# Performance work log

Hardware: AMD Instinct MI355X
Metric: run time of the kernel (lower is better)

Reference implementation:

```python
import jax, jax.numpy as jnp
import numpy as np

N, F, H, C, E = 100000, 128, 64, 16, 1000000


def _prop(x, src, dst, w):
    # gather source features, scale by edge weight, scatter-add to destinations
    msgs = x[src] * w[:, None]  # [E, H]
    return jax.ops.segment_sum(msgs, dst, num_segments=N)


def _gru(x, h, W_ih, W_hh, b_ih, b_hh):
    gi = x @ W_ih.T + b_ih  # [N, 3H]
    gh = h @ W_hh.T + b_hh
    i_r, i_z, i_n = jnp.split(gi, 3, axis=1)
    h_r, h_z, h_n = jnp.split(gh, 3, axis=1)
    r = jax.nn.sigmoid(i_r + h_r)
    z = jax.nn.sigmoid(i_z + h_z)
    n = jnp.tanh(i_n + r * h_n)
    return (1.0 - z) * n + z * h


def setup_inputs() -> dict:
    key = jax.random.key(0)
    ks = jax.random.split(key, 20)
    s = 0.05
    inp = {
        'x': jax.random.normal(ks[0], (N, F), jnp.float32),
        'edge_index': jax.random.randint(ks[1], (2, E), 0, N),
        'edge_weight': jax.random.uniform(ks[2], (E,), jnp.float32),
        'edge_index_re': jax.random.randint(ks[3], (2, E), 0, N),
        'edge_weight_re': jax.random.uniform(ks[4], (E,), jnp.float32),
        'W_first': jax.random.normal(ks[5], (H, F), jnp.float32) * s,
        'b_first': jnp.zeros((H,), jnp.float32),
        'W_con1': jax.random.normal(ks[6], (H, 2 * H), jnp.float32) * s,
        'b_con1': jnp.zeros((H,), jnp.float32),
        'W_con2': jax.random.normal(ks[7], (H, 2 * H), jnp.float32) * s,
        'b_con2': jnp.zeros((H,), jnp.float32),
        'W_lin1': jax.random.normal(ks[8], (H, H), jnp.float32) * s,
        'b_lin1': jnp.zeros((H,), jnp.float32),
        'W_out': jax.random.normal(ks[9], (C, H), jnp.float32) * s,
        'b_out': jnp.zeros((C,), jnp.float32),
        'W_ih': jax.random.normal(ks[10], (3 * H, H), jnp.float32) * s,
        'W_hh': jax.random.normal(ks[11], (3 * H, H), jnp.float32) * s,
        'b_ih': jnp.zeros((3 * H,), jnp.float32),
        'b_hh': jnp.zeros((3 * H,), jnp.float32),
    }
    return inp


def reference(x, edge_index, edge_weight, edge_index_re, edge_weight_re,
              W_first, b_first, W_con1, b_con1, W_con2, b_con2,
              W_lin1, b_lin1, W_out, b_out, W_ih, W_hh, b_ih, b_hh):
    src, dst = edge_index[0], edge_index[1]
    src_r, dst_r = edge_index_re[0], edge_index_re[1]

    x = x @ W_first.T + b_first  # [N, H]; dropout is identity at inference
    h = x

    x1 = _prop(x, src, dst, edge_weight)
    x2 = _prop(x, src_r, dst_r, edge_weight_re)
    x = jnp.concatenate([x1, x2], axis=1) @ W_con1.T + b_con1
    x = _gru(x, h, W_ih, W_hh, b_ih, b_hh)
    x = x @ W_lin1.T + b_lin1

    x1 = _prop(x, src, dst, edge_weight)
    x2 = _prop(x, src_r, dst_r, edge_weight_re)
    x = jnp.concatenate([x1, x2], axis=1) @ W_con2.T + b_con2
    x = _gru(x, h, W_ih, W_hh, b_ih, b_hh)
    x = x @ W_out.T + b_out
    return jax.nn.log_softmax(x, axis=-1)
```

## Files before the change

### kernel.cpp

```cpp
#include <hip/hip_runtime.h>

#define NN 100000
#define FF 128
#define HH 64
#define CC 16
#define EE 1000000
#define NSEG (2*NN)
#define BSH 11
#define BKD  (1 << BSH)
#define NBUK ((NSEG + BKD - 1) / BKD)
#define EPB 4096
#define P1BLK ((2*EE + EPB - 1) / EPB)

typedef __bf16 bf16;
typedef __attribute__((ext_vector_type(8))) __bf16 bf16x8;
typedef __attribute__((ext_vector_type(4))) __bf16 bf16x4;
typedef __attribute__((ext_vector_type(4))) float f32x4;

__device__ __forceinline__ float fsig(float t)  { return 1.0f/(1.0f+__expf(-t)); }
__device__ __forceinline__ float ftanh(float t) { return 1.0f - 2.0f/(__expf(2.0f*t)+1.0f); }

__device__ __forceinline__ unsigned pack_sw(int s, float w) {
    unsigned short u = __builtin_bit_cast(unsigned short, (bf16)w);
    return ((unsigned)s << 15) | (u & 0x7FFFu);
}

__global__ void precomp_kernel(const float* __restrict__ W_ih, const float* __restrict__ b_ih,
                               const float* __restrict__ Wc1,  const float* __restrict__ bc1,
                               const float* __restrict__ Wc2,  const float* __restrict__ bc2,
                               const float* __restrict__ W_hh, const float* __restrict__ W_first,
                               const float* __restrict__ W_lin1, const float* __restrict__ W_out,
                               bf16* __restrict__ W1bf, float* __restrict__ b1,
                               bf16* __restrict__ W2bf, float* __restrict__ b2,
                               bf16* __restrict__ Whbf, bf16* __restrict__ Wfbf,
                               bf16* __restrict__ Wlbf, bf16* __restrict__ Wobf)
{
    int idx = blockIdx.x*blockDim.x + threadIdx.x;
    const int t0 = 192*128;
    const int t1 = t0 + 192;
    const int t2 = t1 + 192*64;
    const int t3 = t2 + 64*128;
    const int t4 = t3 + 64*64;
    const int t5 = t4 + 16*64;
    if (idx < t0) {
        int j = idx >> 7, k = idx & 127;
        float s1 = 0.f, s2 = 0.f;
        for (int m=0; m<64; ++m) {
            float wih = W_ih[j*64+m];
            s1 += wih * Wc1[m*128+k];
            s2 += wih * Wc2[m*128+k];
        }
        W1bf[idx] = (bf16)s1; W2bf[idx] = (bf16)s2;
    } else if (idx < t1) {
        int j = idx - t0;
        float s1 = b_ih[j], s2 = b_ih[j];
        for (int m=0; m<64; ++m) {
            float wih = W_ih[j*64+m];
            s1 += wih * bc1[m];
            s2 += wih * bc2[m];
        }
        b1[j] = s1; b2[j] = s2;
    } else if (idx < t2) {
        int i = idx - t1;  Whbf[i] = (bf16)W_hh[i];
    } else if (idx < t3) {
        int i = idx - t2;  Wfbf[i] = (bf16)W_first[i];
    } else if (idx < t4) {
        int i = idx - t3;  Wlbf[i] = (bf16)W_lin1[i];
    } else if (idx < t5) {
        int i = idx - t4;  Wobf[i] = (bf16)W_out[i];
    }
}


__global__ __launch_bounds__(256) void bucket_count_kernel(const int* __restrict__ ei,
                                                           const int* __restrict__ ei_re,
                                                           int* __restrict__ bkcnt)
{
    __shared__ int hist[NBUK];
    const int t = threadIdx.x;
    for (int i=t; i<NBUK; i+=256) hist[i] = 0;
    __syncthreads();
    const long e0 = (long)blockIdx.x * EPB;
    #pragma unroll
    for (int it=0; it<16; ++it) {
        long e = e0 + it*256 + t;
        int d = -1;
        if (e < EE)        d = ei[EE + e];
        else if (e < 2*EE) d = NN + ei_re[EE + (e - EE)];
        if (d >= 0) atomicAdd(&hist[d >> BSH], 1);
    }
    __syncthreads();
    for (int i=t; i<NBUK; i+=256) if (hist[i]) atomicAdd(&bkcnt[i], hist[i]);
}

__global__ void bucket_scan_kernel(const int* __restrict__ bkcnt,
                                   int* __restrict__ bkbase, int* __restrict__ bkcur,
                                   int* __restrict__ rp)
{
    if (threadIdx.x == 0) {
        int acc = 0;
        for (int i=0; i<NBUK; ++i) { bkbase[i] = acc; bkcur[i] = acc; acc += bkcnt[i]; }
        bkbase[NBUK] = acc;
        rp[NSEG] = 2*EE;
    }
}

__global__ __launch_bounds__(256) void fillA_kernel(const int* __restrict__ ei,
                                                    const float* __restrict__ ew,
                                                    const int* __restrict__ ei_re,
                                                    const float* __restrict__ ew_re,
                                                    int* __restrict__ bkcur,
                                                    int* __restrict__ tmp_d,
                                                    unsigned* __restrict__ tmp_p)
{
    __shared__ int hist[NBUK];
    __shared__ int base[NBUK];
    const int t = threadIdx.x;
    for (int i=t; i<NBUK; i+=256) hist[i] = 0;
    __syncthreads();
    const long e0 = (long)blockIdx.x * EPB;
    int pr[16];
    #pragma unroll
    for (int it=0; it<16; ++it) {
        long e = e0 + it*256 + t;
        int d = -1;
        if (e < EE)        d = ei[EE + e];
        else if (e < 2*EE) d = NN + ei_re[EE + (e - EE)];
        if (d >= 0) {
            int b = d >> BSH;
            int r = atomicAdd(&hist[b], 1);
            pr[it] = (b << 16) | r;
        } else pr[it] = -1;
    }
    __syncthreads();
    for (int i=t; i<NBUK; i+=256) base[i] = atomicAdd(&bkcur[i], hist[i]);
    __syncthreads();
    #pragma unroll
    for (int it=0; it<16; ++it) {
        if (pr[it] < 0) continue;
        long e = e0 + it*256 + t;
        int d, s; float w;
        if (e < EE) { d = ei[EE+e]; s = ei[e]; w = ew[e]; }
        else { long j = e - EE; d = NN + ei_re[EE+j]; s = ei_re[j]; w = ew_re[j]; }
        int pos = base[pr[it] >> 16] + (pr[it] & 0xFFFF);
        tmp_d[pos] = d;
        tmp_p[pos] = pack_sw(s, w);
    }
}

__global__ __launch_bounds__(1024) void fillB_kernel(const int* __restrict__ bkbase,
                                                     const int* __restrict__ tmp_d,
                                                     const unsigned* __restrict__ tmp_p,
                                                     unsigned* __restrict__ edata,
                                                     int* __restrict__ rp)
{
    __shared__ int cntL[BKD];
    __shared__ int scanL[1024];
    const int t  = threadIdx.x;
    const int b  = blockIdx.x;
    const int d0 = b << BSH;
    const int dn = min(BKD, NSEG - d0);
    const int p0 = bkbase[b];
    const int p1 = bkbase[b+1];
    for (int i=t; i<BKD; i+=1024) cntL[i] = 0;
    __syncthreads();
    for (int pos = p0 + t; pos < p1; pos += 1024)
        atomicAdd(&cntL[tmp_d[pos] - d0], 1);
    __syncthreads();
    int a0 = cntL[2*t], a1 = cntL[2*t+1];
    int ps = a0 + a1;
    scanL[t] = ps;
    __syncthreads();
    #pragma unroll
    for (int off=1; off<1024; off<<=1) {
        int x = (t>=off) ? scanL[t-off] : 0;
        __syncthreads();
        scanL[t] += x;
        __syncthreads();
    }
    int g0 = p0 + scanL[t] - ps;
    int g1 = g0 + a0;
    if (2*t   < dn) rp[d0 + 2*t]   = g0;
    if (2*t+1 < dn) rp[d0 + 2*t+1] = g1;
    cntL[2*t]   = g0;
    cntL[2*t+1] = g1;
    __syncthreads();
    for (int pos = p0 + t; pos < p1; pos += 1024) {
        int d = tmp_d[pos];
        int p = atomicAdd(&cntL[d - d0], 1);
        edata[p] = tmp_p[pos];
    }
}

__global__ __launch_bounds__(256) void csr_prop_kernel(const bf16* __restrict__ X,
    const int* __restrict__ rp, const unsigned* __restrict__ edata,
    bf16* __restrict__ x1, bf16* __restrict__ x2)
{
    int s = blockIdx.x*4 + (threadIdx.x>>6);
    if (s >= NSEG) return;
    const int lane = threadIdx.x & 63;
    const int q  = lane >> 4;
    const int fl = lane & 15;
    const int e0 = rp[s], e1 = rp[s+1];
    float a0=0.f, a1=0.f, a2=0.f, a3=0.f;
    for (int base = e0; base < e1; base += 16) {
        unsigned pk[4]; float vw[4];
        #pragma unroll
        for (int j=0;j<4;++j) {
            int e = base + j*4 + q;
            unsigned p = edata[e < e1 ? e : e0];
            pk[j] = p;
            vw[j] = (e < e1) ? __uint_as_float((p & 0x7FFFu) << 16) : 0.f;
        }
        bf16x4 xv[4];
        #pragma unroll
        for (int j=0;j<4;++j)
            xv[j] = *(const bf16x4*)&X[(long)(pk[j] >> 15)*HH + 4*fl];
        #pragma unroll
        for (int j=0;j<4;++j) {
            a0 += vw[j]*(float)xv[j][0];
            a1 += vw[j]*(float)xv[j][1];
            a2 += vw[j]*(float)xv[j][2];
            a3 += vw[j]*(float)xv[j][3];
        }
    }
    a0 += __shfl_xor(a0, 32); a0 += __shfl_xor(a0, 16);
    a1 += __shfl_xor(a1, 32); a1 += __shfl_xor(a1, 16);
    a2 += __shfl_xor(a2, 32); a2 += __shfl_xor(a2, 16);
    a3 += __shfl_xor(a3, 32); a3 += __shfl_xor(a3, 16);
    if (q == 0) {
        bf16* o = (s < NN) ? &x1[(long)s*HH] : &x2[(long)(s-NN)*HH];
        bf16x4 ov = {(bf16)a0, (bf16)a1, (bf16)a2, (bf16)a3};
        *(bf16x4*)&o[4*fl] = ov;
    }
}


__global__ __launch_bounds__(256, 2) void lin_first_mfma_kernel(
    const float* __restrict__ X, const bf16* __restrict__ Wf,
    const float* __restrict__ b, float* __restrict__ Y, bf16* __restrict__ Ybf)
{
    const int t = threadIdx.x;
    const int w = t >> 6, lane = t & 63, col = lane & 15, quad = lane >> 4;
    bf16x8 B[4];
    #pragma unroll
    for (int ks=0; ks<4; ++ks)
        B[ks] = *(const bf16x8*)&Wf[(16*w+col)*128 + ks*32 + quad*8];
    const float bv = b[16*w + col];
    __shared__ bf16 Alds[32][136];
    const int m_st = t >> 3, c_in = t & 7;
    for (int tb = blockIdx.x*32; tb < NN; tb += gridDim.x*32) {
        const float4* rx = (const float4*)&X[(long)(tb+m_st)*FF];
        #pragma unroll
        for (int it=0; it<4; ++it) {
            int cc = c_in + it*8;
            float4 v = rx[cc];
            bf16x4 bvv = {(bf16)v.x,(bf16)v.y,(bf16)v.z,(bf16)v.w};
            *(bf16x4*)&Alds[m_st][cc*4] = bvv;
        }
        __syncthreads();
        f32x4 acc[2] = {{0.f,0.f,0.f,0.f},{0.f,0.f,0.f,0.f}};
        #pragma unroll
        for (int ks=0; ks<4; ++ks)
            #pragma unroll
            for (int mt=0; mt<2; ++mt) {
                bf16x8 a = *(const bf16x8*)&Alds[mt*16+col][ks*32+quad*8];
                acc[mt] = __builtin_amdgcn_mfma_f32_16x16x32_bf16(a, B[ks], acc[mt], 0,0,0);
            }
        __syncthreads();
        #pragma unroll
        for (int mt=0; mt<2; ++mt)
            #pragma unroll
            for (int r=0; r<4; ++r) {
                long n = tb + mt*16 + quad*4 + r;
                float val = acc[mt][r] + bv;
                Y  [n*HH + 16*w+col] = val;
                Ybf[n*HH + 16*w+col] = (bf16)val;
            }
    }
}

__global__ __launch_bounds__(256, 2) void lin64_mfma_kernel(
    const float* __restrict__ X, const bf16* __restrict__ Wl,
    const float* __restrict__ b, bf16* __restrict__ Ybf)
{
    const int t = threadIdx.x;
    const int w = t >> 6, lane = t & 63, col = lane & 15, quad = lane >> 4;
    bf16x8 B[2];
    #pragma unroll
    for (int ks=0; ks<2; ++ks)
        B[ks] = *(const bf16x8*)&Wl[(16*w+col)*64 + ks*32 + quad*8];
    const float bv = b[16*w + col];
    __shared__ bf16 Alds[32][72];
    const int m_st = t >> 3, c_in = t & 7;
    for (int tb = blockIdx.x*32; tb < NN; tb += gridDim.x*32) {
        const float4* rx = (const float4*)&X[(long)(tb+m_st)*HH];
        #pragma unroll
        for (int it=0; it<2; ++it) {
            int cc = c_in + it*8;
            float4 v = rx[cc];
            bf16x4 bvv = {(bf16)v.x,(bf16)v.y,(bf16)v.z,(bf16)v.w};
            *(bf16x4*)&Alds[m_st][cc*4] = bvv;
        }
        __syncthreads();
        f32x4 acc[2] = {{0.f,0.f,0.f,0.f},{0.f,0.f,0.f,0.f}};
        #pragma unroll
        for (int ks=0; ks<2; ++ks)
            #pragma unroll
            for (int mt=0; mt<2; ++mt) {
                bf16x8 a = *(const bf16x8*)&Alds[mt*16+col][ks*32+quad*8];
                acc[mt] = __builtin_amdgcn_mfma_f32_16x16x32_bf16(a, B[ks], acc[mt], 0,0,0);
            }
        __syncthreads();
        #pragma unroll
        for (int mt=0; mt<2; ++mt)
            #pragma unroll
            for (int r=0; r<4; ++r)
                Ybf[(long)(tb+mt*16+quad*4+r)*HH + 16*w+col] = (bf16)(acc[mt][r] + bv);
    }
}

__global__ __launch_bounds__(256) void out_mfma_kernel(
    const float* __restrict__ X, const bf16* __restrict__ Wo,
    const float* __restrict__ b, float* __restrict__ Y)
{
    const int t = threadIdx.x;
    const int w = t >> 6, lane = t & 63, col = lane & 15, quad = lane >> 4;
    bf16x8 B[2];
    #pragma unroll
    for (int ks=0; ks<2; ++ks)
        B[ks] = *(const bf16x8*)&Wo[col*64 + ks*32 + quad*8];
    const float bv = b[col];
    __shared__ bf16 Alds[128][72];
    const int r_st = t >> 1, sub = t & 1;
    const int tb = blockIdx.x*128;
    {
        const float4* rx = (const float4*)&X[(long)(tb+r_st)*HH];
        #pragma unroll
        for (int it=0; it<8; ++it) {
            int cc = sub*8 + it;
            float4 v = rx[cc];
            bf16x4 bvv = {(bf16)v.x,(bf16)v.y,(bf16)v.z,(bf16)v.w};
            *(bf16x4*)&Alds[r_st][cc*4] = bvv;
        }
    }
    __syncthreads();
    f32x4 acc[2] = {{0.f,0.f,0.f,0.f},{0.f,0.f,0.f,0.f}};
    #pragma unroll
    for (int ks=0; ks<2; ++ks)
        #pragma unroll
        for (int mt=0; mt<2; ++mt) {
            bf16x8 a = *(const bf16x8*)&Alds[w*32 + mt*16 + col][ks*32+quad*8];
            acc[mt] = __builtin_amdgcn_mfma_f32_16x16x32_bf16(a, B[ks], acc[mt], 0,0,0);
        }
    #pragma unroll
    for (int mt=0; mt<2; ++mt) {
        #pragma unroll
        for (int r=0; r<4; ++r) {
            int n = tb + w*32 + mt*16 + quad*4 + r;
            float val = acc[mt][r] + bv;
            float m = val;
            #pragma unroll
            for (int off=8; off>0; off>>=1) m = fmaxf(m, __shfl_xor(m, off, 16));
            float ex = __expf(val - m);
            float s = ex;
            #pragma unroll
            for (int off=8; off>0; off>>=1) s += __shfl_xor(s, off, 16);
            if (n < NN) Y[(long)n*CC + col] = val - m - __logf(s);
        }
    }
}

__global__ __launch_bounds__(256, 2) void layer_mfma_kernel(
    const bf16* __restrict__ X1, const bf16* __restrict__ X2,
    const float* __restrict__ H,
    const bf16* __restrict__ Wg, const float* __restrict__ bg,
    const bf16* __restrict__ Wh, const float* __restrict__ bh,
    float* __restrict__ Hout)
{
    const int t    = threadIdx.x;
    const int w    = t >> 6;
    const int lane = t & 63;
    const int col  = lane & 15;
    const int quad = lane >> 4;

    bf16x8 Bg[3][4];
    bf16x8 Bh[3][2];
    float bgv[3], bhv[3];
    #pragma unroll
    for (int jt=0; jt<3; ++jt) {
        int J = jt*64 + 16*w + col;
        #pragma unroll
        for (int ks=0; ks<4; ++ks)
            Bg[jt][ks] = *(const bf16x8*)&Wg[J*128 + ks*32 + quad*8];
        #pragma unroll
        for (int ks=0; ks<2; ++ks)
            Bh[jt][ks] = *(const bf16x8*)&Wh[J*64 + ks*32 + quad*8];
        bgv[jt] = bg[J];
        bhv[jt] = bh[J];
    }

    __shared__ bf16 Alds[32][200];

    const int m_st = t >> 3;
    const int c_in = t & 7;

    for (int tb = blockIdx.x*32; tb < NN; tb += gridDim.x*32) {
        {
            long n = tb + m_st;
            *(bf16x8*)&Alds[m_st][c_in*8]      = *(const bf16x8*)&X1[n*HH + c_in*8];
            *(bf16x8*)&Alds[m_st][64 + c_in*8] = *(const bf16x8*)&X2[n*HH + c_in*8];
            const float4* rh = (const float4*)&H[n*HH];
            float4 a = rh[c_in*2], b4 = rh[c_in*2+1];
            bf16x8 hb = {(bf16)a.x,(bf16)a.y,(bf16)a.z,(bf16)a.w,
                         (bf16)b4.x,(bf16)b4.y,(bf16)b4.z,(bf16)b4.w};
            *(bf16x8*)&Alds[m_st][128 + c_in*8] = hb;
        }
        __syncthreads();

        f32x4 accg[2][3];
        f32x4 acch[2][3];
        #pragma unroll
        for (int mt=0; mt<2; ++mt)
            #pragma unroll
            for (int jt=0; jt<3; ++jt) {
                accg[mt][jt] = (f32x4){0.f,0.f,0.f,0.f};
                acch[mt][jt] = (f32x4){0.f,0.f,0.f,0.f};
            }

        #pragma unroll
        for (int ks=0; ks<4; ++ks) {
            #pragma unroll
            for (int mt=0; mt<2; ++mt) {
                bf16x8 a = *(const bf16x8*)&Alds[mt*16 + col][ks*32 + quad*8];
                #pragma unroll
                for (int jt=0; jt<3; ++jt)
                    accg[mt][jt] = __builtin_amdgcn_mfma_f32_16x16x32_bf16(
                        a, Bg[jt][ks], accg[mt][jt], 0, 0, 0);
            }
        }
        #pragma unroll
        for (int ks=0; ks<2; ++ks) {
            #pragma unroll
            for (int mt=0; mt<2; ++mt) {
                bf16x8 a = *(const bf16x8*)&Alds[mt*16 + col][128 + ks*32 + quad*8];
                #pragma unroll
                for (int jt=0; jt<3; ++jt)
                    acch[mt][jt] = __builtin_amdgcn_mfma_f32_16x16x32_bf16(
                        a, Bh[jt][ks], acch[mt][jt], 0, 0, 0);
            }
        }
        __syncthreads();

        const int c = 16*w + col;
        #pragma unroll
        for (int mt=0; mt<2; ++mt) {
            #pragma unroll
            for (int r=0; r<4; ++r) {
                long n = tb + mt*16 + quad*4 + r;
                float gr = accg[mt][0][r] + bgv[0];
                float gz = accg[mt][1][r] + bgv[1];
                float gn = accg[mt][2][r] + bgv[2];
                float hr = acch[mt][0][r] + bhv[0];
                float hz = acch[mt][1][r] + bhv[1];
                float hn = acch[mt][2][r] + bhv[2];
                float rr = fsig(gr + hr);
                float zz = fsig(gz + hz);
                float nv = ftanh(gn + rr*hn);
                float hv = H[n*HH + c];
                Hout[n*HH + c] = (1.0f - zz)*nv + zz*hv;
            }
        }
    }
}

extern "C" void kernel_launch(void* const* d_in, const int* in_sizes, int n_in,
                              void* d_out, int out_size, void* d_ws, size_t ws_size,
                              hipStream_t stream)
{
    const float* x       = (const float*)d_in[0];
    const int*   ei      = (const int*)  d_in[1];
    const float* ew      = (const float*)d_in[2];
    const int*   ei_re   = (const int*)  d_in[3];
    const float* ew_re   = (const float*)d_in[4];
    const float* W_first = (const float*)d_in[5];
    const float* b_first = (const float*)d_in[6];
    const float* W_con1  = (const float*)d_in[7];
    const float* b_con1  = (const float*)d_in[8];
    const float* W_con2  = (const float*)d_in[9];
    const float* b_con2  = (const float*)d_in[10];
    const float* W_lin1  = (const float*)d_in[11];
    const float* b_lin1  = (const float*)d_in[12];
    const float* W_out   = (const float*)d_in[13];
    const float* b_out   = (const float*)d_in[14];
    const float* W_ih    = (const float*)d_in[15];
    const float* W_hh    = (const float*)d_in[16];
    const float* b_ih    = (const float*)d_in[17];
    const float* b_hh    = (const float*)d_in[18];
    float* out = (float*)d_out;

    float* h    = (float*)d_ws;
    float* hA   = h  + (long)NN*HH;
    bf16*  x1b  = (bf16*)(hA + (long)NN*HH);
    bf16*  x2b  = x1b + (long)NN*HH;
    bf16*  hbf  = x2b + (long)NN*HH;
    bf16*  hAbf = hbf + (long)NN*HH;
    float* b1 = (float*)(hAbf + (long)NN*HH);
    float* b2 = b1 + 192;
    bf16*  W1bf = (bf16*)(b2 + 192);
    bf16*  W2bf = W1bf + 192*128;
    bf16*  Whbf = W2bf + 192*128;
    bf16*  Wfbf = Whbf + 192*64;
    bf16*  Wlbf = Wfbf + 64*128;
    bf16*  Wobf = Wlbf + 64*64;
    int*   rp     = (int*)(Wobf + 16*64);
    int*   bkcnt  = rp + NSEG + 1;
    int*   bkbase = bkcnt + NBUK;
    int*   bkcur  = bkbase + NBUK + 1;
    unsigned* edata = (unsigned*)(bkcur + NBUK);
    int*      tmp_d = (int*)x1b;
    unsigned* tmp_p = (unsigned*)x2b;

    precomp_kernel<<<(192*128 + 192 + 192*64 + 64*128 + 64*64 + 16*64 + 255)/256, 256, 0, stream>>>(
        W_ih, b_ih, W_con1, b_con1, W_con2, b_con2, W_hh, W_first, W_lin1, W_out,
        W1bf, b1, W2bf, b2, Whbf, Wfbf, Wlbf, Wobf);

    hipMemsetAsync(bkcnt, 0, (size_t)NBUK*sizeof(int), stream);
    bucket_count_kernel<<<P1BLK, 256, 0, stream>>>(ei, ei_re, bkcnt);
    bucket_scan_kernel<<<1, 64, 0, stream>>>(bkcnt, bkbase, bkcur, rp);
    fillA_kernel<<<P1BLK, 256, 0, stream>>>(ei, ew, ei_re, ew_re, bkcur, tmp_d, tmp_p);
    fillB_kernel<<<NBUK, 1024, 0, stream>>>(bkbase, tmp_d, tmp_p, edata, rp);

    lin_first_mfma_kernel<<<1024, 256, 0, stream>>>(x, Wfbf, b_first, h, hbf);

    csr_prop_kernel<<<(NSEG + 3)/4, 256, 0, stream>>>(hbf, rp, edata, x1b, x2b);

    layer_mfma_kernel<<<1024, 256, 0, stream>>>(x1b, x2b, h, W1bf, b1, Whbf, b_hh, hA);

    lin64_mfma_kernel<<<1024, 256, 0, stream>>>(hA, Wlbf, b_lin1, hAbf);

    csr_prop_kernel<<<(NSEG + 3)/4, 256, 0, stream>>>(hAbf, rp, edata, x1b, x2b);

    layer_mfma_kernel<<<1024, 256, 0, stream>>>(x1b, x2b, h, W2bf, b2, Whbf, b_hh, hA);

    out_mfma_kernel<<<(NN + 127)/128, 256, 0, stream>>>(hA, Wobf, b_out, out);
}
```

Before: 419.0 us.

## Fuse GRU layer with following linear/log-softmax and streamline CSR gather addressing

The GRU layer kernel now writes its output tile to shared memory as bf16 and immediately applies the next linear (lin1 or the output projection plus log-softmax) with MFMA. This removes the fp32 hA round trip through global memory and two separate kernel launches. The CSR propagation loop is rewritten to use byte-offset addressing derived directly from the packed edge word and packed f32x2 accumulation, which cuts integer work per edge. It also moves edata ahead of rp in the workspace layout. The GRU output is now rounded to bf16 before the follow-up matmul, which adds a small extra precision loss.

```diff
diff --git a/kernel.cpp b/kernel.cpp
--- a/kernel.cpp
+++ b/kernel.cpp
@@ -16,6 +16,7 @@
 typedef __attribute__((ext_vector_type(8))) __bf16 bf16x8;
 typedef __attribute__((ext_vector_type(4))) __bf16 bf16x4;
 typedef __attribute__((ext_vector_type(4))) float f32x4;
+typedef __attribute__((ext_vector_type(2))) float f32x2;
 
 __device__ __forceinline__ float fsig(float t)  { return 1.0f/(1.0f+__expf(-t)); }
 __device__ __forceinline__ float ftanh(float t) { return 1.0f - 2.0f/(__expf(2.0f*t)+1.0f); }
@@ -201,29 +202,31 @@
     const int lane = threadIdx.x & 63;
     const int q  = lane >> 4;
     const int fl = lane & 15;
+    const unsigned foff = 8u*(unsigned)fl;
     const int e0 = rp[s], e1 = rp[s+1];
-    float a0=0.f, a1=0.f, a2=0.f, a3=0.f;
-    for (int base = e0; base < e1; base += 16) {
-        unsigned pk[4]; float vw[4];
-        #pragma unroll
-        for (int j=0;j<4;++j) {
-            int e = base + j*4 + q;
-            unsigned p = edata[e < e1 ? e : e0];
-            pk[j] = p;
-            vw[j] = (e < e1) ? __uint_as_float((p & 0x7FFFu) << 16) : 0.f;
-        }
-        bf16x4 xv[4];
-        #pragma unroll
-        for (int j=0;j<4;++j)
-            xv[j] = *(const bf16x4*)&X[(long)(pk[j] >> 15)*HH + 4*fl];
-        #pragma unroll
-        for (int j=0;j<4;++j) {
-            a0 += vw[j]*(float)xv[j][0];
-            a1 += vw[j]*(float)xv[j][1];
-            a2 += vw[j]*(float)xv[j][2];
-            a3 += vw[j]*(float)xv[j][3];
-        }
-    }
+    const char* Xb = (const char*)X;
+    const char* Eb = (const char*)edata;
+
+    f32x2 acc01 = {0.f, 0.f}, acc23 = {0.f, 0.f};
+    int eq = e0 + q;
+    unsigned eqb = 4u*(unsigned)eq;
+    for (int base = e0; base < e1; base += 16, eq += 16, eqb += 64u) {
+        const int rem = e1 - eq;
+        #pragma unroll
+        for (int j=0; j<4; ++j) {
+            unsigned p = *(const unsigned*)(Eb + (eqb + 16u*(unsigned)j));
+            const bool v = (4*j < rem);
+            float w = v ? __uint_as_float((p & 0x7FFFu) << 16) : 0.f;
+            unsigned voff = v ? (((p >> 8) & 0xFFFFFF80u) | foff) : foff;
+            uint2 d = *(const uint2*)(Xb + voff);
+            f32x2 lo = { __uint_as_float(d.x << 16), __uint_as_float(d.x & 0xFFFF0000u) };
+            f32x2 hi = { __uint_as_float(d.y << 16), __uint_as_float(d.y & 0xFFFF0000u) };
+            f32x2 w2 = { w, w };
+            acc01 += w2 * lo;
+            acc23 += w2 * hi;
+        }
+    }
+    float a0 = acc01.x, a1 = acc01.y, a2 = acc23.x, a3 = acc23.y;
     a0 += __shfl_xor(a0, 32); a0 += __shfl_xor(a0, 16);
     a1 += __shfl_xor(a1, 32); a1 += __shfl_xor(a1, 16);
     a2 += __shfl_xor(a2, 32); a2 += __shfl_xor(a2, 16);
@@ -280,103 +283,14 @@
     }
 }
 
-__global__ __launch_bounds__(256, 2) void lin64_mfma_kernel(
-    const float* __restrict__ X, const bf16* __restrict__ Wl,
-    const float* __restrict__ b, bf16* __restrict__ Ybf)
-{
-    const int t = threadIdx.x;
-    const int w = t >> 6, lane = t & 63, col = lane & 15, quad = lane >> 4;
-    bf16x8 B[2];
-    #pragma unroll
-    for (int ks=0; ks<2; ++ks)
-        B[ks] = *(const bf16x8*)&Wl[(16*w+col)*64 + ks*32 + quad*8];
-    const float bv = b[16*w + col];
-    __shared__ bf16 Alds[32][72];
-    const int m_st = t >> 3, c_in = t & 7;
-    for (int tb = blockIdx.x*32; tb < NN; tb += gridDim.x*32) {
-        const float4* rx = (const float4*)&X[(long)(tb+m_st)*HH];
-        #pragma unroll
-        for (int it=0; it<2; ++it) {
-            int cc = c_in + it*8;
-            float4 v = rx[cc];
-            bf16x4 bvv = {(bf16)v.x,(bf16)v.y,(bf16)v.z,(bf16)v.w};
-            *(bf16x4*)&Alds[m_st][cc*4] = bvv;
-        }
-        __syncthreads();
-        f32x4 acc[2] = {{0.f,0.f,0.f,0.f},{0.f,0.f,0.f,0.f}};
-        #pragma unroll
-        for (int ks=0; ks<2; ++ks)
-            #pragma unroll
-            for (int mt=0; mt<2; ++mt) {
-                bf16x8 a = *(const bf16x8*)&Alds[mt*16+col][ks*32+quad*8];
-                acc[mt] = __builtin_amdgcn_mfma_f32_16x16x32_bf16(a, B[ks], acc[mt], 0,0,0);
-            }
-        __syncthreads();
-        #pragma unroll
-        for (int mt=0; mt<2; ++mt)
-            #pragma unroll
-            for (int r=0; r<4; ++r)
-                Ybf[(long)(tb+mt*16+quad*4+r)*HH + 16*w+col] = (bf16)(acc[mt][r] + bv);
-    }
-}
-
-__global__ __launch_bounds__(256) void out_mfma_kernel(
-    const float* __restrict__ X, const bf16* __restrict__ Wo,
-    const float* __restrict__ b, float* __restrict__ Y)
-{
-    const int t = threadIdx.x;
-    const int w = t >> 6, lane = t & 63, col = lane & 15, quad = lane >> 4;
-    bf16x8 B[2];
-    #pragma unroll
-    for (int ks=0; ks<2; ++ks)
-        B[ks] = *(const bf16x8*)&Wo[col*64 + ks*32 + quad*8];
-    const float bv = b[col];
-    __shared__ bf16 Alds[128][72];
-    const int r_st = t >> 1, sub = t & 1;
-    const int tb = blockIdx.x*128;
-    {
-        const float4* rx = (const float4*)&X[(long)(tb+r_st)*HH];
-        #pragma unroll
-        for (int it=0; it<8; ++it) {
-            int cc = sub*8 + it;
-            float4 v = rx[cc];
-            bf16x4 bvv = {(bf16)v.x,(bf16)v.y,(bf16)v.z,(bf16)v.w};
-            *(bf16x4*)&Alds[r_st][cc*4] = bvv;
-        }
-    }
-    __syncthreads();
-    f32x4 acc[2] = {{0.f,0.f,0.f,0.f},{0.f,0.f,0.f,0.f}};
-    #pragma unroll
-    for (int ks=0; ks<2; ++ks)
-        #pragma unroll
-        for (int mt=0; mt<2; ++mt) {
-            bf16x8 a = *(const bf16x8*)&Alds[w*32 + mt*16 + col][ks*32+quad*8];
-            acc[mt] = __builtin_amdgcn_mfma_f32_16x16x32_bf16(a, B[ks], acc[mt], 0,0,0);
-        }
-    #pragma unroll
-    for (int mt=0; mt<2; ++mt) {
-        #pragma unroll
-        for (int r=0; r<4; ++r) {
-            int n = tb + w*32 + mt*16 + quad*4 + r;
-            float val = acc[mt][r] + bv;
-            float m = val;
-            #pragma unroll
-            for (int off=8; off>0; off>>=1) m = fmaxf(m, __shfl_xor(m, off, 16));
-            float ex = __expf(val - m);
-            float s = ex;
-            #pragma unroll
-            for (int off=8; off>0; off>>=1) s += __shfl_xor(s, off, 16);
-            if (n < NN) Y[(long)n*CC + col] = val - m - __logf(s);
-        }
-    }
-}
-
-__global__ __launch_bounds__(256, 2) void layer_mfma_kernel(
+template<int MODE>
+__global__ __launch_bounds__(256, 2) void layer_fused_kernel(
     const bf16* __restrict__ X1, const bf16* __restrict__ X2,
     const float* __restrict__ H,
     const bf16* __restrict__ Wg, const float* __restrict__ bg,
     const bf16* __restrict__ Wh, const float* __restrict__ bh,
-    float* __restrict__ Hout)
+    const bf16* __restrict__ Ws, const float* __restrict__ bs,
+    bf16* __restrict__ Obf, float* __restrict__ Of)
 {
     const int t    = threadIdx.x;
     const int w    = t >> 6;
@@ -400,7 +314,22 @@
         bhv[jt] = bh[J];
     }
 
+    bf16x8 B2[2];
+    float b2s;
+    if constexpr (MODE == 0) {
+        #pragma unroll
+        for (int ks=0; ks<2; ++ks)
+            B2[ks] = *(const bf16x8*)&Ws[(16*w+col)*64 + ks*32 + quad*8];
+        b2s = bs[16*w + col];
+    } else {
+        #pragma unroll
+        for (int ks=0; ks<2; ++ks)
+            B2[ks] = *(const bf16x8*)&Ws[col*64 + ks*32 + quad*8];
+        b2s = bs[col];
+    }
+
     __shared__ bf16 Alds[32][200];
+    __shared__ bf16 Glds[32][72];
 
     const int m_st = t >> 3;
     const int c_in = t & 7;
@@ -450,7 +379,6 @@
                         a, Bh[jt][ks], acch[mt][jt], 0, 0, 0);
             }
         }
-        __syncthreads();
 
         const int c = 16*w + col;
         #pragma unroll
@@ -468,7 +396,46 @@
                 float zz = fsig(gz + hz);
                 float nv = ftanh(gn + rr*hn);
                 float hv = H[n*HH + c];
-                Hout[n*HH + c] = (1.0f - zz)*nv + zz*hv;
+                Glds[mt*16 + quad*4 + r][c] = (bf16)((1.0f - zz)*nv + zz*hv);
+            }
+        }
+        __syncthreads();
+
+        if constexpr (MODE == 0) {
+            f32x4 acc2[2] = {{0.f,0.f,0.f,0.f},{0.f,0.f,0.f,0.f}};
+            #pragma unroll
+            for (int ks=0; ks<2; ++ks)
+                #pragma unroll
+                for (int mt=0; mt<2; ++mt) {
+                    bf16x8 a = *(const bf16x8*)&Glds[mt*16+col][ks*32+quad*8];
+                    acc2[mt] = __builtin_amdgcn_mfma_f32_16x16x32_bf16(a, B2[ks], acc2[mt], 0,0,0);
+                }
+            #pragma unroll
+            for (int mt=0; mt<2; ++mt)
+                #pragma unroll
+                for (int r=0; r<4; ++r)
+                    Obf[(long)(tb+mt*16+quad*4+r)*HH + 16*w+col] = (bf16)(acc2[mt][r] + b2s);
+        } else {
+            if (w < 2) {
+                f32x4 acc2 = {0.f,0.f,0.f,0.f};
+                #pragma unroll
+                for (int ks=0; ks<2; ++ks) {
+                    bf16x8 a = *(const bf16x8*)&Glds[w*16+col][ks*32+quad*8];
+                    acc2 = __builtin_amdgcn_mfma_f32_16x16x32_bf16(a, B2[ks], acc2, 0,0,0);
+                }
+                #pragma unroll
+                for (int r=0; r<4; ++r) {
+                    long n = tb + w*16 + quad*4 + r;
+                    float val = acc2[r] + b2s;
+                    float m = val;
+                    #pragma unroll
+                    for (int off=8; off>0; off>>=1) m = fmaxf(m, __shfl_xor(m, off, 16));
+                    float ex = __expf(val - m);
+                    float ssum = ex;
+                    #pragma unroll
+                    for (int off=8; off>0; off>>=1) ssum += __shfl_xor(ssum, off, 16);
+                    Of[n*CC + col] = val - m - __logf(ssum);
+                }
             }
         }
     }
@@ -500,8 +467,7 @@
     float* out = (float*)d_out;
 
     float* h    = (float*)d_ws;
-    float* hA   = h  + (long)NN*HH;
-    bf16*  x1b  = (bf16*)(hA + (long)NN*HH);
+    bf16*  x1b  = (bf16*)(h + (long)NN*HH);
     bf16*  x2b  = x1b + (long)NN*HH;
     bf16*  hbf  = x2b + (long)NN*HH;
     bf16*  hAbf = hbf + (long)NN*HH;
@@ -513,11 +479,11 @@
     bf16*  Wfbf = Whbf + 192*64;
     bf16*  Wlbf = Wfbf + 64*128;
     bf16*  Wobf = Wlbf + 64*64;
-    int*   rp     = (int*)(Wobf + 16*64);
+    unsigned* edata = (unsigned*)(Wobf + 16*64);
+    int*   rp     = (int*)(edata + 2*EE);
     int*   bkcnt  = rp + NSEG + 1;
     int*   bkbase = bkcnt + NBUK;
     int*   bkcur  = bkbase + NBUK + 1;
-    unsigned* edata = (unsigned*)(bkcur + NBUK);
     int*      tmp_d = (int*)x1b;
     unsigned* tmp_p = (unsigned*)x2b;
 
@@ -535,13 +501,11 @@
 
     csr_prop_kernel<<<(NSEG + 3)/4, 256, 0, stream>>>(hbf, rp, edata, x1b, x2b);
 
-    layer_mfma_kernel<<<1024, 256, 0, stream>>>(x1b, x2b, h, W1bf, b1, Whbf, b_hh, hA);
-
-    lin64_mfma_kernel<<<1024, 256, 0, stream>>>(hA, Wlbf, b_lin1, hAbf);
+    layer_fused_kernel<0><<<1024, 256, 0, stream>>>(x1b, x2b, h, W1bf, b1, Whbf, b_hh,
+                                                    Wlbf, b_lin1, hAbf, nullptr);
 
     csr_prop_kernel<<<(NSEG + 3)/4, 256, 0, stream>>>(hAbf, rp, edata, x1b, x2b);
 
-    layer_mfma_kernel<<<1024, 256, 0, stream>>>(x1b, x2b, h, W2bf, b2, Whbf, b_hh, hA);
-
-    out_mfma_kernel<<<(NN + 127)/128, 256, 0, stream>>>(hA, Wobf, b_out, out);
-}
+    layer_fused_kernel<1><<<1024, 256, 0, stream>>>(x1b, x2b, h, W2bf, b2, Whbf, b_hh,
+                                                    Wobf, b_out, nullptr, out);
+}
```

New measurement: 391.8 us. -6.5%, faster.
